# Kernel tuning notes

Measured on AMD Instinct MI355X. Metric: run time of the kernel, lower is better.

The kernel has to match this reference:

```python
import jax, jax.numpy as jnp
import numpy as np

N = 1024
E = 16384
F_IN = 128
H = 64
ALPHA = 0.7


def _gcn(x, src, dst, W, b):
    # PyG GCNConv: add self-loops, symmetric deg^{-1/2} normalization, aggregate at dst.
    loop = jnp.arange(N)
    s = jnp.concatenate([src, loop])
    d = jnp.concatenate([dst, loop])
    deg = jax.ops.segment_sum(jnp.ones_like(s, jnp.float32), d, num_segments=N)
    dinv = jnp.where(deg > 0, jax.lax.rsqrt(deg), 0.0)
    norm = dinv[s] * dinv[d]  # [E+N]
    h = x @ W  # [N,H]
    out = jax.ops.segment_sum(norm[:, None] * h[s], d, num_segments=N)
    return out + b


def _gat(x, src, dst, ew, W, a_src, a_dst, w_edge, a_edge, b):
    # PyG GATConv (heads=1) with scalar edge_attr via lin_edge(edge_dim=1).
    h = x @ W  # [N,H]
    al_s = h @ a_src  # [N]
    al_d = h @ a_dst  # [N]
    loop = jnp.arange(N)
    s = jnp.concatenate([src, loop])
    d = jnp.concatenate([dst, loop])
    ew_l = jnp.concatenate([ew, jnp.full((N,), jnp.mean(ew))])  # fill_value='mean' for self-loops
    c = jnp.dot(w_edge, a_edge)  # scalar: (lin_edge(ew) * att_edge).sum() = ew * c
    e = jax.nn.leaky_relu(al_s[s] + al_d[d] + ew_l * c, 0.2)  # [E+N]
    # segment softmax over destination nodes (every node has a self-loop -> no empty segments)
    emax = jax.ops.segment_max(e, d, num_segments=N)
    ex = jnp.exp(e - emax[d])
    denom = jax.ops.segment_sum(ex, d, num_segments=N)
    alpha = ex / denom[d]
    out = jax.ops.segment_sum(alpha[:, None] * h[s], d, num_segments=N)
    return out + b


def setup_inputs() -> dict:
    key = jax.random.key(0)
    ks = jax.random.split(key, 24)
    g = lambda k, shape, fan: jax.random.normal(k, shape, jnp.float32) / np.sqrt(fan)
    inp = {
        "x": jax.random.normal(ks[0], (N, F_IN), jnp.float32),
        "edge_index_above": jax.random.randint(ks[1], (2, E), 0, N),
        "edge_index_distance": jax.random.randint(ks[2], (2, E), 0, N),
        "edge_weights_distance": jax.random.uniform(ks[3], (E,), jnp.float32),
        # GCNConv1 / GATConv1 (in 128 -> 64)
        "W_gcn1": g(ks[4], (F_IN, H), F_IN), "b_gcn1": jnp.zeros((H,), jnp.float32),
        "W_gat1": g(ks[5], (F_IN, H), F_IN), "att_src1": g(ks[6], (H,), H),
        "att_dst1": g(ks[7], (H,), H), "w_edge1": g(ks[8], (H,), 1),
        "att_edge1": g(ks[9], (H,), H), "b_gat1": jnp.zeros((H,), jnp.float32),
        # GCNConv2 / GATConv2 (64 -> 64)
        "W_gcn2": g(ks[10], (H, H), H), "b_gcn2": jnp.zeros((H,), jnp.float32),
        "W_gat2": g(ks[11], (H, H), H), "att_src2": g(ks[12], (H,), H),
        "att_dst2": g(ks[13], (H,), H), "w_edge2": g(ks[14], (H,), 1),
        "att_edge2": g(ks[15], (H,), H), "b_gat2": jnp.zeros((H,), jnp.float32),
        # GCNConv3 (64 -> 64)
        "W_gcn3": g(ks[16], (H, H), H), "b_gcn3": jnp.zeros((H,), jnp.float32),
        # predictor MLP: Linear(128,64) -> ReLU -> Linear(64,1) -> Sigmoid
        "Wp1": g(ks[17], (2 * H, H), 2 * H), "bp1": jnp.zeros((H,), jnp.float32),
        "Wp2": g(ks[18], (H, 1), H), "bp2": jnp.zeros((1,), jnp.float32),
    }
    return inp


def reference(x, edge_index_above, edge_index_distance, edge_weights_distance,
              W_gcn1, b_gcn1, W_gat1, att_src1, att_dst1, w_edge1, att_edge1, b_gat1,
              W_gcn2, b_gcn2, W_gat2, att_src2, att_dst2, w_edge2, att_edge2, b_gat2,
              W_gcn3, b_gcn3, Wp1, bp1, Wp2, bp2):
    sa, da = edge_index_above[0], edge_index_above[1]
    sd, dd = edge_index_distance[0], edge_index_distance[1]
    ew = edge_weights_distance

    xa1 = jax.nn.relu(_gcn(x, sa, da, W_gcn1, b_gcn1))
    xd1 = jax.nn.relu(_gat(x, sd, dd, ew, W_gat1, att_src1, att_dst1, w_edge1, att_edge1, b_gat1))
    xa2 = jax.nn.relu(_gcn(xa1, sa, da, W_gcn2, b_gcn2))
    xd2 = jax.nn.relu(_gat(xd1, sd, dd, ew, W_gat2, att_src2, att_dst2, w_edge2, att_edge2, b_gat2))
    xc = ALPHA * xa2 + (1.0 - ALPHA) * xd2
    h = jax.nn.relu(_gcn(xc, sa, da, W_gcn3, b_gcn3))  # [N,H]

    # All-pairs predictor, fused: concat([h_i, h_j]) @ Wp1 = h_i @ Wp1[:H] + h_j @ Wp1[H:]
    h1 = h @ Wp1[:H]  # [N,H] contribution of start node
    h2 = h @ Wp1[H:]  # [N,H] contribution of end node
    pre = jax.nn.relu(h1[:, None, :] + h2[None, :, :] + bp1)  # [N,N,H]
    logits = jnp.einsum('ijh,h->ij', pre, Wp2[:, 0]) + bp2[0]  # [N,N]
    return jax.nn.sigmoid(logits).reshape(-1)  # [N*N], row-major = cartesian_prod order
```

## Files before the change

### kernel.cpp

```cpp
#include <hip/hip_runtime.h>

constexpr int NV  = 1024;
constexpr int EV  = 16384;
constexpr int FIN = 128;
constexpr int HD  = 64;
constexpr int CAP = 64;

__device__ __forceinline__ float relu_(float v){ return fmaxf(v, 0.f); }

struct KArgs {
    const float* x;
    const int *sa, *da, *sd, *dd;
    const float* ew;
    const float *Wg1, *bg1;
    const float *Wt1, *as1, *ad1, *we1, *ae1, *bt1;
    const float *Wg2, *bg2;
    const float *Wt2, *as2, *ad2, *we2, *ae2, *bt2;
    const float *Wg3, *bg3;
    const float *Wp1, *bp1, *Wp2, *bp2;
    int *cnt_a, *cnt_d;
    float* scal;
    float *al_s1, *al_d1, *al_s2, *al_d2;
    int *ell_a, *ell_d;
    float* ellw_d;
    float *hg1, *hga1, *hg2, *hga2, *hg3, *h1, *h2;
    float* out;
};

__device__ __forceinline__ float gcn_row(const KArgs& A, const float* __restrict__ h,
                                         const float* __restrict__ bias, int d, int k)
{
    int deg = min(A.cnt_a[d], CAP);
    float dv  = rsqrtf((float)deg + 1.f);
    float acc = dv * h[d*HD + k];
    const int* row = A.ell_a + d*CAP;
    int p = 0;
    float a0=0.f, a1=0.f, a2=0.f, a3=0.f;
    for (; p + 4 <= deg; p += 4) {
        int s0=row[p], s1=row[p+1], s2=row[p+2], s3=row[p+3];
        a0 = fmaf(rsqrtf((float)A.cnt_a[s0]+1.f), h[s0*HD + k], a0);
        a1 = fmaf(rsqrtf((float)A.cnt_a[s1]+1.f), h[s1*HD + k], a1);
        a2 = fmaf(rsqrtf((float)A.cnt_a[s2]+1.f), h[s2*HD + k], a2);
        a3 = fmaf(rsqrtf((float)A.cnt_a[s3]+1.f), h[s3*HD + k], a3);
    }
    for (; p < deg; ++p) {
        int s = row[p];
        a0 = fmaf(rsqrtf((float)A.cnt_a[s]+1.f), h[s*HD + k], a0);
    }
    acc += (a0+a1) + (a2+a3);
    return relu_(fmaf(dv, acc, bias[k]));
}

__device__ __forceinline__ float gat_row(const KArgs& A, const float* __restrict__ h,
                                         const float* __restrict__ bias,
                                         float c, float ewm, int d, int k)
{
    int deg = min(A.cnt_d[d], CAP);
    float aD = A.al_d1[0];
    (void)aD;
    return 0.f;
}

template<bool L2>
__device__ __forceinline__ float gat_row_t(const KArgs& A, const float* __restrict__ h,
                                           const float* __restrict__ bias,
                                           const float* __restrict__ al_s,
                                           const float* __restrict__ al_d,
                                           float c, float ewm, int d, int k)
{
    int deg = min(A.cnt_d[d], CAP);
    float aD = al_d[d];
    float es = al_s[d] + aD + ewm*c;
    es = expf((es > 0.f) ? es : 0.2f*es);
    float num = es * h[d*HD + k];
    float den = es;
    const int*   row  = A.ell_d  + d*CAP;
    const float* wrow = A.ellw_d + d*CAP;
    int p = 0;
    for (; p + 2 <= deg; p += 2) {
        int s0 = row[p], s1 = row[p+1];
        float e0 = al_s[s0] + aD + wrow[p]*c;
        float e1 = al_s[s1] + aD + wrow[p+1]*c;
        float x0 = expf((e0 > 0.f) ? e0 : 0.2f*e0);
        float x1 = expf((e1 > 0.f) ? e1 : 0.2f*e1);
        den += x0 + x1;
        num = fmaf(x0, h[s0*HD + k], num);
        num = fmaf(x1, h[s1*HD + k], num);
    }
    for (; p < deg; ++p) {
        int s = row[p];
        float e = al_s[s] + aD + wrow[p]*c;
        float ex = expf((e > 0.f) ? e : 0.2f*e);
        den += ex;
        num = fmaf(ex, h[s*HD + k], num);
    }
    return relu_(num/den + bias[k]);
}

__device__ __forceinline__ float mm_row_lds(const float4* __restrict__ rowF4,
                                            const float* __restrict__ Wf, int j)
{
    float acc = 0.f;
    #pragma unroll
    for (int k4 = 0; k4 < 16; k4++) {
        float4 r = rowF4[k4];
        acc = fmaf(r.x, Wf[(4*k4+0)*64 + j], acc);
        acc = fmaf(r.y, Wf[(4*k4+1)*64 + j], acc);
        acc = fmaf(r.z, Wf[(4*k4+2)*64 + j], acc);
        acc = fmaf(r.w, Wf[(4*k4+3)*64 + j], acc);
    }
    return acc;
}

__global__ __launch_bounds__(256) void k1(KArgs A)
{
    __shared__ __align__(16) float4 Ws[FIN*16];
    const int b = blockIdx.x, tid = threadIdx.x;
    if (b < 512) {
        bool gcn = (b < 256);
        const float4* Wsrc = (const float4*)(gcn ? A.Wg1 : A.Wt1);
        for (int r = tid; r < FIN*16; r += 256) Ws[r] = Wsrc[r];
        __syncthreads();
        int t = (gcn ? b : b-256)*256 + tid, i = t >> 6, j = t & 63;
        const float4* xr = (const float4*)(A.x + i*FIN);
        const float*  Wf = (const float*)Ws;
        float acc = 0.f;
        #pragma unroll
        for (int k4 = 0; k4 < FIN/4; k4++) {
            float4 xv = xr[k4];
            acc = fmaf(xv.x, Wf[(4*k4+0)*64 + j], acc);
            acc = fmaf(xv.y, Wf[(4*k4+1)*64 + j], acc);
            acc = fmaf(xv.z, Wf[(4*k4+2)*64 + j], acc);
            acc = fmaf(xv.w, Wf[(4*k4+3)*64 + j], acc);
        }
        if (gcn) {
            A.hg1[t] = acc;
        } else {
            A.hga1[t] = acc;
            float ps = acc * A.as1[j];
            float pd = acc * A.ad1[j];
            for (int off = 32; off; off >>= 1) {
                ps += __shfl_down(ps, off, 64);
                pd += __shfl_down(pd, off, 64);
            }
            if (j == 0) { A.al_s1[i] = ps; A.al_d1[i] = pd; }
        }
    } else if (b < 576) {
        int e = (b-512)*256 + tid;
        int dA = A.da[e], dD = A.dd[e];
        int pa = atomicAdd(&A.cnt_a[dA], 1);
        if (pa < CAP) A.ell_a[dA*CAP + pa] = A.sa[e];
        float w = A.ew[e];
        int pd = atomicAdd(&A.cnt_d[dD], 1);
        if (pd < CAP) { A.ell_d[dD*CAP + pd] = A.sd[e]; A.ellw_d[dD*CAP + pd] = w; }
        for (int off = 32; off; off >>= 1) w += __shfl_down(w, off, 64);
        if ((tid & 63) == 0) atomicAdd(&A.scal[3], w);
    } else {
        if (tid < 64) {
            float p1 = A.we1[tid]*A.ae1[tid];
            float p2 = A.we2[tid]*A.ae2[tid];
            for (int off = 32; off; off >>= 1) {
                p1 += __shfl_down(p1, off, 64);
                p2 += __shfl_down(p2, off, 64);
            }
            if (tid == 0) { A.scal[1] = p1; A.scal[2] = p2; }
        }
    }
}

__global__ __launch_bounds__(256) void k2(KArgs A)
{
    __shared__ __align__(16) float4 Ws[HD*16];
    __shared__ float rowb[4*64];
    const int b = blockIdx.x, tid = threadIdx.x;
    const float4* Wsrc = (const float4*)((b < 256) ? A.Wg2 : A.Wt2);
    for (int r = tid; r < HD*16; r += 256) Ws[r] = Wsrc[r];
    __syncthreads();
    int w = tid >> 6, k = tid & 63;
    const float* Wf = (const float*)Ws;
    if (b < 256) {
        int d = b*4 + w;
        rowb[w*64 + k] = gcn_row(A, A.hg1, A.bg1, d, k);
        A.hg2[d*HD + k] = mm_row_lds((const float4*)(rowb + w*64), Wf, k);
    } else {
        int i = (b-256)*4 + w;
        float c = A.scal[1], ewm = A.scal[3] * (1.f/EV);
        rowb[w*64 + k] = gat_row_t<false>(A, A.hga1, A.bt1, A.al_s1, A.al_d1,
                                          c, ewm, i, k);
        float acc = mm_row_lds((const float4*)(rowb + w*64), Wf, k);
        A.hga2[i*HD + k] = acc;
        float ps = acc * A.as2[k];
        float pd = acc * A.ad2[k];
        for (int off = 32; off; off >>= 1) {
            ps += __shfl_down(ps, off, 64);
            pd += __shfl_down(pd, off, 64);
        }
        if (k == 0) { A.al_s2[i] = ps; A.al_d2[i] = pd; }
    }
}

__global__ __launch_bounds__(256) void k3(KArgs A)
{
    __shared__ __align__(16) float4 Ws[HD*16];
    __shared__ float rows[4*64];
    const int b = blockIdx.x, tid = threadIdx.x;
    for (int r = tid; r < HD*16; r += 256) Ws[r] = ((const float4*)A.Wg3)[r];
    int w = tid >> 6, k = tid & 63;
    int node = b*2 + (w >> 1);
    float v;
    if ((w & 1) == 0) {
        v = 0.7f * gcn_row(A, A.hg2, A.bg2, node, k);
    } else {
        float c = A.scal[2], ewm = A.scal[3] * (1.f/EV);
        v = 0.3f * gat_row_t<true>(A, A.hga2, A.bt2, A.al_s2, A.al_d2,
                                   c, ewm, node, k);
    }
    rows[w*64 + k] = v;
    __syncthreads();
    if ((w & 1) == 0) {
        const float* Wf = (const float*)Ws;
        const float4* r0 = (const float4*)(rows + w*64);
        const float4* r1 = (const float4*)(rows + (w+1)*64);
        float acc = 0.f;
        #pragma unroll
        for (int k4 = 0; k4 < 16; k4++) {
            float4 ra = r0[k4], rb = r1[k4];
            acc = fmaf(ra.x+rb.x, Wf[(4*k4+0)*64 + k], acc);
            acc = fmaf(ra.y+rb.y, Wf[(4*k4+1)*64 + k], acc);
            acc = fmaf(ra.z+rb.z, Wf[(4*k4+2)*64 + k], acc);
            acc = fmaf(ra.w+rb.w, Wf[(4*k4+3)*64 + k], acc);
        }
        A.hg3[node*HD + k] = acc;
    }
}

__global__ __launch_bounds__(256) void k4(KArgs A)
{
    __shared__ __align__(16) float4 Wp[FIN*16];
    __shared__ float rowb[4*64];
    const int b = blockIdx.x, tid = threadIdx.x;
    for (int r = tid; r < FIN*16; r += 256) Wp[r] = ((const float4*)A.Wp1)[r];
    __syncthreads();
    int w = tid >> 6, k = tid & 63;
    int d = b*4 + w;
    rowb[w*64 + k] = gcn_row(A, A.hg3, A.bg3, d, k);
    const float*  Wf = (const float*)Wp;
    const float4* rF = (const float4*)(rowb + w*64);
    float a1 = 0.f, a2 = 0.f;
    #pragma unroll
    for (int k4i = 0; k4i < 16; k4i++) {
        float4 r = rF[k4i];
        a1 = fmaf(r.x, Wf[(4*k4i+0)*64 + k], a1);
        a2 = fmaf(r.x, Wf[(64+4*k4i+0)*64 + k], a2);
        a1 = fmaf(r.y, Wf[(4*k4i+1)*64 + k], a1);
        a2 = fmaf(r.y, Wf[(64+4*k4i+1)*64 + k], a2);
        a1 = fmaf(r.z, Wf[(4*k4i+2)*64 + k], a1);
        a2 = fmaf(r.z, Wf[(64+4*k4i+2)*64 + k], a2);
        a1 = fmaf(r.w, Wf[(4*k4i+3)*64 + k], a1);
        a2 = fmaf(r.w, Wf[(64+4*k4i+3)*64 + k], a2);
    }
    A.h1[d*HD + k] = a1 + A.bp1[k];
    A.h2[d*HD + k] = a2;
}

__global__ __launch_bounds__(256) void k5(KArgs A)
{
    __shared__ float4 s1[32*17], s2[32*17], w2s[16];
    const int tid = threadIdx.x;
    int by = blockIdx.x >> 5, bx = blockIdx.x & 31;
    int i0 = by*32, j0 = bx*32;
    for (int r = tid; r < 512; r += 256) {
        int row = r >> 4, c = r & 15;
        s1[row*17 + c] = ((const float4*)A.h1)[(i0+row)*16 + c];
        s2[row*17 + c] = ((const float4*)A.h2)[(j0+row)*16 + c];
    }
    if (tid < 16) w2s[tid] = ((const float4*)A.Wp2)[tid];
    __syncthreads();
    int ty = tid >> 4, tx = tid & 15;
    float a00=0.f, a01=0.f, a10=0.f, a11=0.f;
    #pragma unroll
    for (int k4 = 0; k4 < 16; k4++) {
        float4 va0 = s1[ty*17 + k4],      va1 = s1[(ty+16)*17 + k4];
        float4 vb0 = s2[tx*17 + k4],      vb1 = s2[(tx+16)*17 + k4];
        float4 wv  = w2s[k4];
#define STEP(c) \
        a00 = fmaf(fmaxf(va0.c+vb0.c, 0.f), wv.c, a00); \
        a01 = fmaf(fmaxf(va0.c+vb1.c, 0.f), wv.c, a01); \
        a10 = fmaf(fmaxf(va1.c+vb0.c, 0.f), wv.c, a10); \
        a11 = fmaf(fmaxf(va1.c+vb1.c, 0.f), wv.c, a11);
        STEP(x) STEP(y) STEP(z) STEP(w)
#undef STEP
    }
    float bb = A.bp2[0];
    int i = i0 + ty, jj = j0 + tx;
    A.out[i*NV + jj]            = 1.f/(1.f + expf(-(a00+bb)));
    A.out[i*NV + jj + 16]       = 1.f/(1.f + expf(-(a01+bb)));
    A.out[(i+16)*NV + jj]       = 1.f/(1.f + expf(-(a10+bb)));
    A.out[(i+16)*NV + jj + 16]  = 1.f/(1.f + expf(-(a11+bb)));
}

extern "C" void kernel_launch(void* const* d_in, const int* in_sizes, int n_in,
                              void* d_out, int out_size, void* d_ws, size_t ws_size,
                              hipStream_t stream)
{
    KArgs A;
    A.x   = (const float*)d_in[0];
    const int* ei_a = (const int*)d_in[1];
    const int* ei_d = (const int*)d_in[2];
    A.ew  = (const float*)d_in[3];
    A.Wg1 = (const float*)d_in[4];  A.bg1 = (const float*)d_in[5];
    A.Wt1 = (const float*)d_in[6];  A.as1 = (const float*)d_in[7];
    A.ad1 = (const float*)d_in[8];  A.we1 = (const float*)d_in[9];
    A.ae1 = (const float*)d_in[10]; A.bt1 = (const float*)d_in[11];
    A.Wg2 = (const float*)d_in[12]; A.bg2 = (const float*)d_in[13];
    A.Wt2 = (const float*)d_in[14]; A.as2 = (const float*)d_in[15];
    A.ad2 = (const float*)d_in[16]; A.we2 = (const float*)d_in[17];
    A.ae2 = (const float*)d_in[18]; A.bt2 = (const float*)d_in[19];
    A.Wg3 = (const float*)d_in[20]; A.bg3 = (const float*)d_in[21];
    A.Wp1 = (const float*)d_in[22]; A.bp1 = (const float*)d_in[23];
    A.Wp2 = (const float*)d_in[24]; A.bp2 = (const float*)d_in[25];
    A.sa = ei_a;      A.da = ei_a + EV;
    A.sd = ei_d;      A.dd = ei_d + EV;
    A.out = (float*)d_out;

    float* W = (float*)d_ws;
    A.cnt_a  = (int*)(W + 0);
    A.cnt_d  = (int*)(W + 1024);
    A.scal   = W + 2048;
    A.al_s1  = W + 2064;
    A.al_d1  = W + 3088;
    A.al_s2  = W + 4112;
    A.al_d2  = W + 5136;
    A.ell_a  = (int*)(W + 6160);
    A.ell_d  = (int*)(W + 71696);
    A.ellw_d = W + 137232;
    A.hg1    = W + 202768;
    A.hga1   = W + 268304;
    A.hg2    = W + 333840;
    A.hga2   = W + 399376;
    A.hg3    = W + 464912;
    A.h1     = W + 530448;
    A.h2     = W + 595984;

    hipMemsetAsync(d_ws, 0, 2064*sizeof(float), stream);

    k1<<<577,  256, 0, stream>>>(A);
    k2<<<512,  256, 0, stream>>>(A);
    k3<<<512,  256, 0, stream>>>(A);
    k4<<<256,  256, 0, stream>>>(A);
    k5<<<1024, 256, 0, stream>>>(A);
}
```

Measured before the change: 150.1 us.

## Fuse all stages into one cooperative persistent kernel with grid syncs

Replaces the five separate kernel launches with a single cooperative kernel of 256 blocks. Each stage walks its work items in a grid-stride loop, and stages are separated by grid.sync(). The goal is to remove launch gaps and inter-kernel drain between the dependent GNN stages. In exchange, each block reloads weights per work unit and has less parallelism per stage than the original grids. If the cooperative launch fails, the old five-kernel path is used.

```diff
diff --git a/kernel.cpp b/kernel.cpp
--- a/kernel.cpp
+++ b/kernel.cpp
@@ -1,10 +1,14 @@
 #include <hip/hip_runtime.h>
+#include <hip/hip_cooperative_groups.h>
+
+namespace cg = cooperative_groups;
 
 constexpr int NV  = 1024;
 constexpr int EV  = 16384;
 constexpr int FIN = 128;
 constexpr int HD  = 64;
 constexpr int CAP = 64;
+constexpr int GRID = 256;
 
 __device__ __forceinline__ float relu_(float v){ return fmaxf(v, 0.f); }
 
@@ -53,20 +57,9 @@
 
 __device__ __forceinline__ float gat_row(const KArgs& A, const float* __restrict__ h,
                                          const float* __restrict__ bias,
+                                         const float* __restrict__ al_s,
+                                         const float* __restrict__ al_d,
                                          float c, float ewm, int d, int k)
-{
-    int deg = min(A.cnt_d[d], CAP);
-    float aD = A.al_d1[0];
-    (void)aD;
-    return 0.f;
-}
-
-template<bool L2>
-__device__ __forceinline__ float gat_row_t(const KArgs& A, const float* __restrict__ h,
-                                           const float* __restrict__ bias,
-                                           const float* __restrict__ al_s,
-                                           const float* __restrict__ al_d,
-                                           float c, float ewm, int d, int k)
 {
     int deg = min(A.cnt_d[d], CAP);
     float aD = al_d[d];
@@ -112,6 +105,191 @@
     return acc;
 }
 
+__global__ __launch_bounds__(256) void fused(KArgs A)
+{
+    __shared__ __align__(16) unsigned char smem[33792];
+    float4*      WsF4 = (float4*)smem;
+    const float* Wsf  = (const float*)smem;
+    float*       rowb = (float*)(smem + 32768);
+
+    cg::grid_group grid = cg::this_grid();
+    const int b = blockIdx.x, tid = threadIdx.x;
+    const int w = tid >> 6, k = tid & 63;
+    const int G = gridDim.x;
+
+    for (int e = b*256 + tid; e < EV; e += G*256) {
+        int dA = A.da[e], dD = A.dd[e];
+        int pa = atomicAdd(&A.cnt_a[dA], 1);
+        if (pa < CAP) A.ell_a[dA*CAP + pa] = A.sa[e];
+        float wv = A.ew[e];
+        int pd = atomicAdd(&A.cnt_d[dD], 1);
+        if (pd < CAP) { A.ell_d[dD*CAP + pd] = A.sd[e]; A.ellw_d[dD*CAP + pd] = wv; }
+        for (int off = 32; off; off >>= 1) wv += __shfl_down(wv, off, 64);
+        if ((tid & 63) == 0) atomicAdd(&A.scal[3], wv);
+    }
+    if (b == 0 && tid < 64) {
+        float p1 = A.we1[tid]*A.ae1[tid];
+        float p2 = A.we2[tid]*A.ae2[tid];
+        for (int off = 32; off; off >>= 1) {
+            p1 += __shfl_down(p1, off, 64);
+            p2 += __shfl_down(p2, off, 64);
+        }
+        if (tid == 0) { A.scal[1] = p1; A.scal[2] = p2; }
+    }
+    for (int u = b; u < 512; u += G) {
+        bool gcn = (u < 256);
+        const float4* Wsrc = (const float4*)(gcn ? A.Wg1 : A.Wt1);
+        __syncthreads();
+        for (int r = tid; r < FIN*16; r += 256) WsF4[r] = Wsrc[r];
+        __syncthreads();
+        int t = (gcn ? u : u-256)*256 + tid, i = t >> 6, j = t & 63;
+        const float4* xr = (const float4*)(A.x + i*FIN);
+        float acc = 0.f;
+        #pragma unroll
+        for (int k4 = 0; k4 < FIN/4; k4++) {
+            float4 xv = xr[k4];
+            acc = fmaf(xv.x, Wsf[(4*k4+0)*64 + j], acc);
+            acc = fmaf(xv.y, Wsf[(4*k4+1)*64 + j], acc);
+            acc = fmaf(xv.z, Wsf[(4*k4+2)*64 + j], acc);
+            acc = fmaf(xv.w, Wsf[(4*k4+3)*64 + j], acc);
+        }
+        if (gcn) {
+            A.hg1[t] = acc;
+        } else {
+            A.hga1[t] = acc;
+            float ps = acc * A.as1[j];
+            float pd = acc * A.ad1[j];
+            for (int off = 32; off; off >>= 1) {
+                ps += __shfl_down(ps, off, 64);
+                pd += __shfl_down(pd, off, 64);
+            }
+            if (j == 0) { A.al_s1[i] = ps; A.al_d1[i] = pd; }
+        }
+    }
+    grid.sync();
+
+    for (int u = b; u < 512; u += G) {
+        bool gcnp = (u < 256);
+        const float4* Wsrc = (const float4*)(gcnp ? A.Wg2 : A.Wt2);
+        __syncthreads();
+        for (int r = tid; r < HD*16; r += 256) WsF4[r] = Wsrc[r];
+        __syncthreads();
+        if (gcnp) {
+            int d = u*4 + w;
+            rowb[w*64 + k] = gcn_row(A, A.hg1, A.bg1, d, k);
+            A.hg2[d*HD + k] = mm_row_lds((const float4*)(rowb + w*64), Wsf, k);
+        } else {
+            int i = (u-256)*4 + w;
+            float c = A.scal[1], ewm = A.scal[3] * (1.f/EV);
+            rowb[w*64 + k] = gat_row(A, A.hga1, A.bt1, A.al_s1, A.al_d1,
+                                     c, ewm, i, k);
+            float acc = mm_row_lds((const float4*)(rowb + w*64), Wsf, k);
+            A.hga2[i*HD + k] = acc;
+            float ps = acc * A.as2[k];
+            float pd = acc * A.ad2[k];
+            for (int off = 32; off; off >>= 1) {
+                ps += __shfl_down(ps, off, 64);
+                pd += __shfl_down(pd, off, 64);
+            }
+            if (k == 0) { A.al_s2[i] = ps; A.al_d2[i] = pd; }
+        }
+    }
+    grid.sync();
+
+    for (int r = tid; r < HD*16; r += 256) WsF4[r] = ((const float4*)A.Wg3)[r];
+    for (int u = b; u < 512; u += G) {
+        int node = u*2 + (w >> 1);
+        float v;
+        if ((w & 1) == 0) {
+            v = 0.7f * gcn_row(A, A.hg2, A.bg2, node, k);
+        } else {
+            float c = A.scal[2], ewm = A.scal[3] * (1.f/EV);
+            v = 0.3f * gat_row(A, A.hga2, A.bt2, A.al_s2, A.al_d2,
+                               c, ewm, node, k);
+        }
+        rowb[w*64 + k] = v;
+        __syncthreads();
+        if ((w & 1) == 0) {
+            const float4* r0 = (const float4*)(rowb + w*64);
+            const float4* r1 = (const float4*)(rowb + (w+1)*64);
+            float acc = 0.f;
+            #pragma unroll
+            for (int k4 = 0; k4 < 16; k4++) {
+                float4 ra = r0[k4], rb = r1[k4];
+                acc = fmaf(ra.x+rb.x, Wsf[(4*k4+0)*64 + k], acc);
+                acc = fmaf(ra.y+rb.y, Wsf[(4*k4+1)*64 + k], acc);
+                acc = fmaf(ra.z+rb.z, Wsf[(4*k4+2)*64 + k], acc);
+                acc = fmaf(ra.w+rb.w, Wsf[(4*k4+3)*64 + k], acc);
+            }
+            A.hg3[node*HD + k] = acc;
+        }
+        __syncthreads();
+    }
+    grid.sync();
+
+    for (int r = tid; r < FIN*16; r += 256) WsF4[r] = ((const float4*)A.Wp1)[r];
+    __syncthreads();
+    for (int u = b; u < 256; u += G) {
+        int d = u*4 + w;
+        rowb[w*64 + k] = gcn_row(A, A.hg3, A.bg3, d, k);
+        const float4* rF = (const float4*)(rowb + w*64);
+        float a1 = 0.f, a2 = 0.f;
+        #pragma unroll
+        for (int k4i = 0; k4i < 16; k4i++) {
+            float4 r = rF[k4i];
+            a1 = fmaf(r.x, Wsf[(4*k4i+0)*64 + k], a1);
+            a2 = fmaf(r.x, Wsf[(64+4*k4i+0)*64 + k], a2);
+            a1 = fmaf(r.y, Wsf[(4*k4i+1)*64 + k], a1);
+            a2 = fmaf(r.y, Wsf[(64+4*k4i+1)*64 + k], a2);
+            a1 = fmaf(r.z, Wsf[(4*k4i+2)*64 + k], a1);
+            a2 = fmaf(r.z, Wsf[(64+4*k4i+2)*64 + k], a2);
+            a1 = fmaf(r.w, Wsf[(4*k4i+3)*64 + k], a1);
+            a2 = fmaf(r.w, Wsf[(64+4*k4i+3)*64 + k], a2);
+        }
+        A.h1[d*HD + k] = a1 + A.bp1[k];
+        A.h2[d*HD + k] = a2;
+    }
+    grid.sync();
+
+    {
+        float4* s1  = (float4*)smem;
+        float4* s2  = (float4*)(smem + 8704);
+        float4* w2s = (float4*)(smem + 17408);
+        for (int t = b; t < 1024; t += G) {
+            __syncthreads();
+            int i0 = (t >> 5) * 32, j0 = (t & 31) * 32;
+            for (int r = tid; r < 512; r += 256) {
+                int row = r >> 4, c = r & 15;
+                s1[row*17 + c] = ((const float4*)A.h1)[(i0+row)*16 + c];
+                s2[row*17 + c] = ((const float4*)A.h2)[(j0+row)*16 + c];
+            }
+            if (tid < 16) w2s[tid] = ((const float4*)A.Wp2)[tid];
+            __syncthreads();
+            int ty = tid >> 4, tx = tid & 15;
+            float a00=0.f, a01=0.f, a10=0.f, a11=0.f;
+            #pragma unroll
+            for (int k4 = 0; k4 < 16; k4++) {
+                float4 va0 = s1[ty*17 + k4],      va1 = s1[(ty+16)*17 + k4];
+                float4 vb0 = s2[tx*17 + k4],      vb1 = s2[(tx+16)*17 + k4];
+                float4 wv  = w2s[k4];
+#define STEP(c) \
+                a00 = fmaf(fmaxf(va0.c+vb0.c, 0.f), wv.c, a00); \
+                a01 = fmaf(fmaxf(va0.c+vb1.c, 0.f), wv.c, a01); \
+                a10 = fmaf(fmaxf(va1.c+vb0.c, 0.f), wv.c, a10); \
+                a11 = fmaf(fmaxf(va1.c+vb1.c, 0.f), wv.c, a11);
+                STEP(x) STEP(y) STEP(z) STEP(w)
+#undef STEP
+            }
+            float bb = A.bp2[0];
+            int i = i0 + ty, jj = j0 + tx;
+            A.out[i*NV + jj]            = 1.f/(1.f + expf(-(a00+bb)));
+            A.out[i*NV + jj + 16]       = 1.f/(1.f + expf(-(a01+bb)));
+            A.out[(i+16)*NV + jj]       = 1.f/(1.f + expf(-(a10+bb)));
+            A.out[(i+16)*NV + jj + 16]  = 1.f/(1.f + expf(-(a11+bb)));
+        }
+    }
+}
+
 __global__ __launch_bounds__(256) void k1(KArgs A)
 {
     __shared__ __align__(16) float4 Ws[FIN*16];
@@ -150,11 +328,11 @@
         int dA = A.da[e], dD = A.dd[e];
         int pa = atomicAdd(&A.cnt_a[dA], 1);
         if (pa < CAP) A.ell_a[dA*CAP + pa] = A.sa[e];
-        float w = A.ew[e];
+        float wv = A.ew[e];
         int pd = atomicAdd(&A.cnt_d[dD], 1);
-        if (pd < CAP) { A.ell_d[dD*CAP + pd] = A.sd[e]; A.ellw_d[dD*CAP + pd] = w; }
-        for (int off = 32; off; off >>= 1) w += __shfl_down(w, off, 64);
-        if ((tid & 63) == 0) atomicAdd(&A.scal[3], w);
+        if (pd < CAP) { A.ell_d[dD*CAP + pd] = A.sd[e]; A.ellw_d[dD*CAP + pd] = wv; }
+        for (int off = 32; off; off >>= 1) wv += __shfl_down(wv, off, 64);
+        if ((tid & 63) == 0) atomicAdd(&A.scal[3], wv);
     } else {
         if (tid < 64) {
             float p1 = A.we1[tid]*A.ae1[tid];
@@ -185,8 +363,8 @@
     } else {
         int i = (b-256)*4 + w;
         float c = A.scal[1], ewm = A.scal[3] * (1.f/EV);
-        rowb[w*64 + k] = gat_row_t<false>(A, A.hga1, A.bt1, A.al_s1, A.al_d1,
-                                          c, ewm, i, k);
+        rowb[w*64 + k] = gat_row(A, A.hga1, A.bt1, A.al_s1, A.al_d1,
+                                 c, ewm, i, k);
         float acc = mm_row_lds((const float4*)(rowb + w*64), Wf, k);
         A.hga2[i*HD + k] = acc;
         float ps = acc * A.as2[k];
@@ -212,8 +390,7 @@
         v = 0.7f * gcn_row(A, A.hg2, A.bg2, node, k);
     } else {
         float c = A.scal[2], ewm = A.scal[3] * (1.f/EV);
-        v = 0.3f * gat_row_t<true>(A, A.hga2, A.bt2, A.al_s2, A.al_d2,
-                                   c, ewm, node, k);
+        v = 0.3f * gat_row(A, A.hga2, A.bt2, A.al_s2, A.al_d2, c, ewm, node, k);
     }
     rows[w*64 + k] = v;
     __syncthreads();
@@ -344,9 +521,16 @@
 
     hipMemsetAsync(d_ws, 0, 2064*sizeof(float), stream);
 
-    k1<<<577,  256, 0, stream>>>(A);
-    k2<<<512,  256, 0, stream>>>(A);
-    k3<<<512,  256, 0, stream>>>(A);
-    k4<<<256,  256, 0, stream>>>(A);
-    k5<<<1024, 256, 0, stream>>>(A);
-}
+    void* kargs[] = { (void*)&A };
+    hipError_t rc = hipLaunchCooperativeKernel(
+        reinterpret_cast<const void*>(fused), dim3(GRID), dim3(256),
+        kargs, 0u, stream);
+    if (rc != hipSuccess) {
+        (void)hipGetLastError();
+        k1<<<577,  256, 0, stream>>>(A);
+        k2<<<512,  256, 0, stream>>>(A);
+        k3<<<512,  256, 0, stream>>>(A);
+        k4<<<256,  256, 0, stream>>>(A);
+        k5<<<1024, 256, 0, stream>>>(A);
+    }
+}
```

Result: slower. 305.7 us (+103.7%).
